# Optimization experiments

Hardware: AMD Instinct MI355X
Metric: run time of the kernel (lower is better)

## Reference

```python
import jax, jax.numpy as jnp
import numpy as np

E = 16        # n_routed_experts
K = 2         # n_activated_experts (top-k)
DIM = 1024    # model dim
INTER = 704   # moe_inter_dim
B, S = 4, 1024


def setup_inputs() -> dict:
    key = jax.random.key(0)
    ks = jax.random.split(key, 5)
    x = jax.random.normal(ks[0], (B, S, DIM), dtype=jnp.float32)
    Wg = jax.random.normal(ks[1], (E, DIM), dtype=jnp.float32) * 0.02   # gate (Linear, no bias)
    W1 = jax.random.normal(ks[2], (E, DIM, INTER), dtype=jnp.float32) * 0.02
    W3 = jax.random.normal(ks[3], (E, DIM, INTER), dtype=jnp.float32) * 0.02
    W2 = jax.random.normal(ks[4], (E, INTER, DIM), dtype=jnp.float32) * 0.02
    return {"x": x, "Wg": Wg, "W1": W1, "W2": W2, "W3": W3}


def reference(x, Wg, W1, W2, W3):
    # Single-process semantics of MoEWithAll2All: the all2all dispatch/combine is
    # pure communication; the math is: softmax router -> top-k -> renormalize ->
    # per-expert SwiGLU MLP on routed tokens -> weighted combine at original slots.
    Bb, Ss, D = x.shape
    xf = x.reshape(-1, D)                              # [N, D], N = B*S
    logits = xf @ Wg.T                                 # [N, E]
    probs = jax.nn.softmax(logits, axis=-1)
    topw, topi = jax.lax.top_k(probs, K)               # [N, K]
    topw = topw / topw.sum(axis=-1, keepdims=True)
    # gates[n, e] = routed weight of token n for expert e (0 if not routed):
    # identical math to the masked gather/scatter dispatch in the original.
    gates = (jax.nn.one_hot(topi, E, dtype=xf.dtype) * topw[..., None]).sum(axis=1)  # [N, E]
    out = jnp.zeros_like(xf)
    for e in range(E):                                 # small fixed loop over experts
        h = jax.nn.silu(xf @ W1[e]) * (xf @ W3[e])     # SwiGLU expert, [N, INTER]
        out = out + gates[:, e:e + 1] * (h @ W2[e])    # combine with gate weights
    return out.reshape(Bb, Ss, D)
```

## Files before the change

### kernel.cpp

```cpp
#include <hip/hip_runtime.h>

#define NTOK 4096
#define DDIM 1024
#define IDIM 704
#define NEXP 16
#define NSLOT 8192
#define MAXT 128
#define NPAD1 768
#define WTBLK 4480

typedef __attribute__((ext_vector_type(8))) short bf16x8;
typedef __attribute__((ext_vector_type(4))) float f32x4;
typedef __attribute__((ext_vector_type(4))) unsigned short us4;
typedef __attribute__((ext_vector_type(8))) unsigned short us8;

__device__ __forceinline__ unsigned short f2bf(float f) {
  union { float f; unsigned int u; } v; v.f = f;
  unsigned int r = v.u + 0x7fffu + ((v.u >> 16) & 1u);
  return (unsigned short)(r >> 16);
}

__device__ __forceinline__ float bf2f(unsigned short b) {
  union { unsigned int u; float f; } v; v.u = ((unsigned int)b) << 16;
  return v.f;
}

__device__ __forceinline__ void gload_lds16(const void* g, void* l) {
  __builtin_amdgcn_global_load_lds((const __attribute__((address_space(1))) void*)g,
                                   (__attribute__((address_space(3))) void*)l, 16, 0, 0);
}

__global__ void k_front(const float* __restrict__ x, const float* __restrict__ Wg,
                        const float* __restrict__ W1, const float* __restrict__ W3,
                        const float* __restrict__ W2, int* __restrict__ tok_e,
                        float* __restrict__ tok_w, unsigned short* __restrict__ Xb,
                        unsigned short* __restrict__ W1T, unsigned short* __restrict__ W3T,
                        unsigned short* __restrict__ W2T) {
  int b = blockIdx.x;
  if (b < WTBLK) {
    __shared__ unsigned short lds[2][64 * 64];
    const float* src; unsigned short* dst;
    int ksz, nsz, kx, np, e;
    if (b < 3072) {
      int which = (b >= 1536) ? 1 : 0;
      int tb = b - which * 1536;
      kx = tb & 15; int rest = tb >> 4; np = rest % 6; e = rest / 6;
      ksz = DDIM; nsz = IDIM;
      src = (which ? W3 : W1) + (size_t)e * DDIM * IDIM;
      dst = (which ? W3T : W1T) + (size_t)e * NPAD1 * DDIM;
    } else {
      int tb = b - 3072;
      kx = tb % 11; int rest = tb / 11; np = rest & 7; e = rest >> 3;
      ksz = IDIM; nsz = DDIM;
      src = W2 + (size_t)e * IDIM * DDIM;
      dst = W2T + (size_t)e * DDIM * IDIM;
    }
    int k0 = kx * 64;
    int t = threadIdx.x;
    int kr4 = (t >> 4) * 4, nc4 = (t & 15) * 4;
    int n0a = np * 128, n0b = n0a + 64;
    bool bvalid = n0b < nsz;
    f32x4 v0[4], v1[4];
#pragma unroll
    for (int j = 0; j < 4; ++j)
      v0[j] = *(const f32x4*)(src + (size_t)(k0 + kr4 + j) * nsz + n0a + nc4);
    if (bvalid) {
#pragma unroll
      for (int j = 0; j < 4; ++j)
        v1[j] = *(const f32x4*)(src + (size_t)(k0 + kr4 + j) * nsz + n0b + nc4);
    }
    int c8 = kr4 >> 3, half = (kr4 >> 2) & 1;
#pragma unroll
    for (int i = 0; i < 4; ++i) {
      int row = nc4 + i;
      int addr = row * 64 + ((c8 ^ ((row >> 2) & 7)) << 3) + half * 4;
      us4 o0;
#pragma unroll
      for (int j = 0; j < 4; ++j) o0[j] = f2bf(v0[j][i]);
      *(us4*)(lds[0] + addr) = o0;
      if (bvalid) {
        us4 o1;
#pragma unroll
        for (int j = 0; j < 4; ++j) o1[j] = f2bf(v1[j][i]);
        *(us4*)(lds[1] + addr) = o1;
      }
    }
    __syncthreads();
    int nr = t >> 3, kc8 = t & 7;
#pragma unroll
    for (int q = 0; q < 2; ++q) {
      int row = nr + q * 32;
      us8 oA = *(const us8*)(lds[0] + row * 64 + ((kc8 ^ ((row >> 2) & 7)) << 3));
      *(us8*)(dst + (size_t)(n0a + row) * ksz + k0 + kc8 * 8) = oA;
      us8 oB = bvalid ? *(const us8*)(lds[1] + row * 64 + ((kc8 ^ ((row >> 2) & 7)) << 3))
                      : (us8)(unsigned short)0;
      *(us8*)(dst + (size_t)(n0b + row) * ksz + k0 + kc8 * 8) = oB;
    }
    return;
  }
  int rb = b - WTBLK;
  int lane = threadIdx.x & 63;
  int wv = threadIdx.x >> 6;
  int tk = rb * 4 + wv;
  const f32x4* xr = (const f32x4*)(x + (size_t)tk * DDIM);
  us4* xbr = (us4*)(Xb + (size_t)tk * DDIM);
  f32x4 xv[4];
#pragma unroll
  for (int c = 0; c < 4; ++c) {
    xv[c] = xr[c * 64 + lane];
    us4 o;
#pragma unroll
    for (int j = 0; j < 4; ++j) o[j] = f2bf(xv[c][j]);
    xbr[c * 64 + lane] = o;
  }
  float p[NEXP];
#pragma unroll
  for (int e = 0; e < NEXP; ++e) {
    const f32x4* wr = (const f32x4*)(Wg + (size_t)e * DDIM);
    float s = 0.f;
#pragma unroll
    for (int c = 0; c < 4; ++c) {
      f32x4 w4 = wr[c * 64 + lane];
      s += xv[c][0]*w4[0] + xv[c][1]*w4[1] + xv[c][2]*w4[2] + xv[c][3]*w4[3];
    }
    p[e] = s;
  }
#pragma unroll
  for (int off = 32; off >= 1; off >>= 1) {
#pragma unroll
    for (int e = 0; e < NEXP; ++e) p[e] += __shfl_xor(p[e], off);
  }
  int i0 = 0; float b0 = p[0];
#pragma unroll
  for (int e = 1; e < NEXP; ++e) if (p[e] > b0) { b0 = p[e]; i0 = e; }
  int i1 = -1; float b1 = -3.4e38f;
#pragma unroll
  for (int e = 0; e < NEXP; ++e) if (e != i0 && p[e] > b1) { b1 = p[e]; i1 = e; }
  if (lane == 0) {
    float w0 = 1.f / (1.f + __expf(b1 - b0));
    tok_e[2*tk] = i0; tok_e[2*tk+1] = i1;
    tok_w[2*tk] = w0; tok_w[2*tk+1] = 1.f - w0;
  }
}

__global__ void k_scan_scatter(const int* __restrict__ tok_e, const float* __restrict__ tok_w,
                               int* __restrict__ counts, int* __restrict__ offsets,
                               int* __restrict__ ntiles, int* __restrict__ tile_e,
                               int* __restrict__ tile_m0, int* __restrict__ token_map,
                               float* __restrict__ gate_w, int* __restrict__ slot_of) {
  int eb = blockIdx.x;
  int t = threadIdx.x, lane = t & 63, wv = t >> 6;
  __shared__ unsigned long long masks[4][32];
  __shared__ int wcnt[4][NEXP];
  __shared__ int counts_s[NEXP];
  int ce[NEXP];
#pragma unroll
  for (int e = 0; e < NEXP; ++e) ce[e] = 0;
#pragma unroll 1
  for (int s = 0; s < 32; ++s) {
    int te = tok_e[wv * 2048 + s * 64 + lane];
#pragma unroll
    for (int e = 0; e < NEXP; ++e) {
      unsigned long long m = __ballot(te == e);
      ce[e] += (int)__popcll(m);
      if (e == eb && lane == 0) masks[wv][s] = m;
    }
  }
  if (lane == 0) {
#pragma unroll
    for (int e = 0; e < NEXP; ++e) wcnt[wv][e] = ce[e];
  }
  __syncthreads();
  if (t < NEXP) {
    int s = wcnt[0][t] + wcnt[1][t] + wcnt[2][t] + wcnt[3][t];
    counts_s[t] = s;
    if (eb == 0) counts[t] = s;
  }
  __syncthreads();
  if (eb == 0 && t == 0) {
    int acc = 0, nt = 0;
    for (int e = 0; e < NEXP; ++e) {
      offsets[e] = acc;
      int cc = counts_s[e];
      for (int m0 = 0; m0 < cc; m0 += 128) { tile_e[nt] = e; tile_m0[nt] = m0; ++nt; }
      acc += cc;
    }
    offsets[NEXP] = acc;
    *ntiles = nt;
  }
  int run = 0;
  for (int e = 0; e < eb; ++e) run += counts_s[e];
  for (int w = 0; w < wv; ++w) run += wcnt[w][eb];
  unsigned long long below = (lane == 63) ? 0x7fffffffffffffffull : ((1ull << lane) - 1ull);
#pragma unroll 1
  for (int s = 0; s < 32; ++s) {
    unsigned long long m = masks[wv][s];
    if ((m >> lane) & 1ull) {
      int i = wv * 2048 + s * 64 + lane;
      int slot = run + (int)__popcll(m & below);
      token_map[slot] = i >> 1;
      gate_w[slot] = tok_w[i];
      slot_of[i] = slot;
    }
    run += (int)__popcll(m);
  }
}

__global__ __launch_bounds__(256, 2)
void k_gemm1(const unsigned short* __restrict__ Xb, const unsigned short* __restrict__ W1T,
             const unsigned short* __restrict__ W3T, const int* __restrict__ token_map,
             const float* __restrict__ gate_w, const int* __restrict__ ntiles,
             const int* __restrict__ tile_e, const int* __restrict__ tile_m0,
             const int* __restrict__ offsets, const int* __restrict__ counts,
             unsigned short* __restrict__ H) {
  int idx = blockIdx.x;
  int xcd = idx & 7, r = idx >> 3;
  int g = (r >> 2) * 8 + xcd;
  int mm = r & 3;
  int ty = (g / 6) * 4 + mm;
  if (ty >= *ntiles) return;
  int n0 = (g % 6) * 128;
  int e = tile_e[ty], m0 = tile_m0[ty];
  int base_slot = offsets[e] + m0;
  int cnt = counts[e] - m0; if (cnt > 128) cnt = 128;

  __shared__ unsigned short As[2][128 * 32];
  __shared__ unsigned short B1s[2][128 * 32];
  __shared__ unsigned short B3s[2][128 * 32];

  int t = threadIdx.x;
  int row = t >> 2, kc = (t & 3) * 8;
  int r0i = base_slot + row;      if (r0i > NSLOT - 1) r0i = NSLOT - 1;
  int r1i = base_slot + 64 + row; if (r1i > NSLOT - 1) r1i = NSLOT - 1;
  const unsigned short* ag0 = Xb + (size_t)token_map[r0i] * DDIM + kc;
  const unsigned short* ag1 = Xb + (size_t)token_map[r1i] * DDIM + kc;
  const unsigned short* b1g0 = W1T + ((size_t)e * NPAD1 + n0 + row) * DDIM + kc;
  const unsigned short* b1g1 = b1g0 + (size_t)64 * DDIM;
  const unsigned short* b3g0 = W3T + ((size_t)e * NPAD1 + n0 + row) * DDIM + kc;
  const unsigned short* b3g1 = b3g0 + (size_t)64 * DDIM;
  int d0 = t * 8, d1 = 2048 + t * 8;

  int lane = t & 63, wv = t >> 6;
  int wm = (wv >> 1) * 64, wn = (wv & 1) * 64;
  int lm = lane & 15, kg = lane >> 4;
  int ao[4], bo[4];
#pragma unroll
  for (int i = 0; i < 4; ++i) {
    ao[i] = (wm + i * 16 + lm) * 32 + kg * 8;
    bo[i] = (wn + i * 16 + lm) * 32 + kg * 8;
  }

  f32x4 acc1[4][4], acc3[4][4];
#pragma unroll
  for (int i = 0; i < 4; ++i)
#pragma unroll
    for (int j = 0; j < 4; ++j) { acc1[i][j] = 0.f; acc3[i][j] = 0.f; }

  gload_lds16(ag0, As[0] + d0);
  gload_lds16(ag1, As[0] + d1);
  gload_lds16(b1g0, B1s[0] + d0);
  gload_lds16(b1g1, B1s[0] + d1);
  gload_lds16(b3g0, B3s[0] + d0);
  gload_lds16(b3g1, B3s[0] + d1);

  for (int k0 = 0; k0 < DDIM; k0 += 32) {
    int cur = (k0 >> 5) & 1;
    __syncthreads();
    if (k0 + 32 < DDIM) {
      int nx = cur ^ 1, kn = k0 + 32;
      gload_lds16(ag0 + kn, As[nx] + d0);
      gload_lds16(ag1 + kn, As[nx] + d1);
      gload_lds16(b1g0 + kn, B1s[nx] + d0);
      gload_lds16(b1g1 + kn, B1s[nx] + d1);
      gload_lds16(b3g0 + kn, B3s[nx] + d0);
      gload_lds16(b3g1 + kn, B3s[nx] + d1);
    }
    bf16x8 av[4], b1v[4], b3v[4];
#pragma unroll
    for (int i = 0; i < 4; ++i) {
      av[i]  = *(const bf16x8*)(As[cur] + ao[i]);
      b1v[i] = *(const bf16x8*)(B1s[cur] + bo[i]);
      b3v[i] = *(const bf16x8*)(B3s[cur] + bo[i]);
    }
#pragma unroll
    for (int mi = 0; mi < 4; ++mi)
#pragma unroll
      for (int ni = 0; ni < 4; ++ni) {
        acc1[mi][ni] = __builtin_amdgcn_mfma_f32_16x16x32_bf16(av[mi], b1v[ni], acc1[mi][ni], 0, 0, 0);
        acc3[mi][ni] = __builtin_amdgcn_mfma_f32_16x16x32_bf16(av[mi], b3v[ni], acc3[mi][ni], 0, 0, 0);
      }
  }

#pragma unroll
  for (int mi = 0; mi < 4; ++mi)
#pragma unroll
    for (int rr = 0; rr < 4; ++rr) {
      int orow = wm + mi * 16 + kg * 4 + rr;
      if (orow < cnt) {
        int slot = base_slot + orow;
        float gw = gate_w[slot];
        unsigned short* hrow = H + (size_t)slot * IDIM;
#pragma unroll
        for (int ni = 0; ni < 4; ++ni) {
          int nn = n0 + wn + ni * 16 + lm;
          if (nn < IDIM) {
            float v1 = acc1[mi][ni][rr];
            float v3 = acc3[mi][ni][rr];
            float hh = v1 / (1.f + __expf(-v1)) * v3 * gw;
            hrow[nn] = f2bf(hh);
          }
        }
      }
    }
}

__global__ __launch_bounds__(256, 3)
void k_gemm2(const unsigned short* __restrict__ H, const unsigned short* __restrict__ W2T,
             const int* __restrict__ ntiles, const int* __restrict__ tile_e,
             const int* __restrict__ tile_m0, const int* __restrict__ offsets,
             const int* __restrict__ counts, unsigned short* __restrict__ O2) {
  int idx = blockIdx.x;
  int xcd = idx & 7, r = idx >> 3;
  int g = (r >> 2) * 8 + xcd;
  int mm = r & 3;
  int ty = (g >> 3) * 4 + mm;
  if (ty >= *ntiles) return;
  int n0 = (g & 7) * 128;
  int e = tile_e[ty], m0 = tile_m0[ty];
  int base_slot = offsets[e] + m0;
  int cnt = counts[e] - m0; if (cnt > 128) cnt = 128;

  __shared__ unsigned short As[2][128 * 32];
  __shared__ unsigned short Bs[2][128 * 32];

  int t = threadIdx.x;
  int row = t >> 2, kc = (t & 3) * 8;
  int r0i = base_slot + row;      if (r0i > NSLOT - 1) r0i = NSLOT - 1;
  int r1i = base_slot + 64 + row; if (r1i > NSLOT - 1) r1i = NSLOT - 1;
  const unsigned short* ag0 = H + (size_t)r0i * IDIM + kc;
  const unsigned short* ag1 = H + (size_t)r1i * IDIM + kc;
  const unsigned short* bg0 = W2T + ((size_t)e * DDIM + n0 + row) * IDIM + kc;
  const unsigned short* bg1 = bg0 + (size_t)64 * IDIM;
  int d0 = t * 8, d1 = 2048 + t * 8;

  int lane = t & 63, wv = t >> 6;
  int wm = (wv >> 1) * 64, wn = (wv & 1) * 64;
  int lm = lane & 15, kg = lane >> 4;
  int ao[4], bo[4];
#pragma unroll
  for (int i = 0; i < 4; ++i) {
    ao[i] = (wm + i * 16 + lm) * 32 + kg * 8;
    bo[i] = (wn + i * 16 + lm) * 32 + kg * 8;
  }

  f32x4 acc[4][4];
#pragma unroll
  for (int i = 0; i < 4; ++i)
#pragma unroll
    for (int j = 0; j < 4; ++j) acc[i][j] = 0.f;

  gload_lds16(ag0, As[0] + d0);
  gload_lds16(ag1, As[0] + d1);
  gload_lds16(bg0, Bs[0] + d0);
  gload_lds16(bg1, Bs[0] + d1);

  for (int k0 = 0; k0 < IDIM; k0 += 32) {
    int cur = (k0 >> 5) & 1;
    __syncthreads();
    if (k0 + 32 < IDIM) {
      int nx = cur ^ 1, kn = k0 + 32;
      gload_lds16(ag0 + kn, As[nx] + d0);
      gload_lds16(ag1 + kn, As[nx] + d1);
      gload_lds16(bg0 + kn, Bs[nx] + d0);
      gload_lds16(bg1 + kn, Bs[nx] + d1);
    }
    bf16x8 av[4], bv[4];
#pragma unroll
    for (int i = 0; i < 4; ++i) {
      av[i] = *(const bf16x8*)(As[cur] + ao[i]);
      bv[i] = *(const bf16x8*)(Bs[cur] + bo[i]);
    }
#pragma unroll
    for (int mi = 0; mi < 4; ++mi)
#pragma unroll
      for (int ni = 0; ni < 4; ++ni)
        acc[mi][ni] = __builtin_amdgcn_mfma_f32_16x16x32_bf16(av[mi], bv[ni], acc[mi][ni], 0, 0, 0);
  }

#pragma unroll
  for (int mi = 0; mi < 4; ++mi)
#pragma unroll
    for (int rr = 0; rr < 4; ++rr) {
      int orow = wm + mi * 16 + kg * 4 + rr;
      if (orow < cnt) {
        unsigned short* op = O2 + (size_t)(base_slot + orow) * DDIM + n0;
#pragma unroll
        for (int ni = 0; ni < 4; ++ni)
          op[wn + ni * 16 + lm] = f2bf(acc[mi][ni][rr]);
      }
    }
}

__global__ void k_combine(const unsigned short* __restrict__ O2, const int* __restrict__ slot_of,
                          float* __restrict__ out) {
  int tk = blockIdx.x, tt = threadIdx.x;
  int s0 = slot_of[2 * tk], s1 = slot_of[2 * tk + 1];
  us4 a = ((const us4*)(O2 + (size_t)s0 * DDIM))[tt];
  us4 b = ((const us4*)(O2 + (size_t)s1 * DDIM))[tt];
  f32x4 o;
#pragma unroll
  for (int j = 0; j < 4; ++j) o[j] = bf2f(a[j]) + bf2f(b[j]);
  ((f32x4*)(out + (size_t)tk * DDIM))[tt] = o;
}

extern "C" void kernel_launch(void* const* d_in, const int* in_sizes, int n_in,
                              void* d_out, int out_size, void* d_ws, size_t ws_size,
                              hipStream_t stream) {
  const float* x  = (const float*)d_in[0];
  const float* Wg = (const float*)d_in[1];
  const float* W1 = (const float*)d_in[2];
  const float* W2 = (const float*)d_in[3];
  const float* W3 = (const float*)d_in[4];
  float* out = (float*)d_out;

  char* ws = (char*)d_ws;
  size_t off = 0;
  unsigned short* Xb = (unsigned short*)(ws + off); off += (size_t)NTOK * DDIM * 2;
  unsigned short* H  = (unsigned short*)(ws + off); off += (size_t)NSLOT * IDIM * 2;
  unsigned short* O2 = (unsigned short*)(ws + off); off += (size_t)NSLOT * DDIM * 2;
  unsigned short* W1T = (unsigned short*)(ws + off); off += (size_t)NEXP * NPAD1 * DDIM * 2;
  unsigned short* W3T = (unsigned short*)(ws + off); off += (size_t)NEXP * NPAD1 * DDIM * 2;
  unsigned short* W2T = (unsigned short*)(ws + off); off += (size_t)NEXP * DDIM * IDIM * 2;
  int* counts  = (int*)(ws + off); off += 64;
  int* offsets = (int*)(ws + off); off += 128;
  int* ntiles  = (int*)(ws + off); off += 64;
  int* tile_e  = (int*)(ws + off); off += MAXT * 4;
  int* tile_m0 = (int*)(ws + off); off += MAXT * 4;
  int* tok_e   = (int*)(ws + off); off += NSLOT * 4;
  float* tok_w = (float*)(ws + off); off += NSLOT * 4;
  int* token_map = (int*)(ws + off); off += NSLOT * 4;
  float* gate_w  = (float*)(ws + off); off += NSLOT * 4;
  int* slot_of   = (int*)(ws + off); off += NSLOT * 4;

  k_front<<<WTBLK + 1024, 256, 0, stream>>>(x, Wg, W1, W3, W2, tok_e, tok_w, Xb,
                                            W1T, W3T, W2T);
  k_scan_scatter<<<NEXP, 256, 0, stream>>>(tok_e, tok_w, counts, offsets, ntiles,
                                           tile_e, tile_m0, token_map, gate_w, slot_of);
  k_gemm1<<<480, 256, 0, stream>>>(Xb, W1T, W3T, token_map, gate_w, ntiles, tile_e,
                                   tile_m0, offsets, counts, H);
  k_gemm2<<<640, 256, 0, stream>>>(H, W2T, ntiles, tile_e, tile_m0, offsets, counts, O2);
  k_combine<<<4096, 256, 0, stream>>>(O2, slot_of, out);
}
```

Before: 297.8 us.

## Widen weight-transpose tiles, route two tokens per wave, bit-ballot expert counting

```diff
diff --git a/kernel.cpp b/kernel.cpp
--- a/kernel.cpp
+++ b/kernel.cpp
@@ -7,7 +7,8 @@
 #define NSLOT 8192
 #define MAXT 128
 #define NPAD1 768
-#define WTBLK 4480
+#define RTRBLK 512
+#define TRBLK 2240
 
 typedef __attribute__((ext_vector_type(8))) short bf16x8;
 typedef __attribute__((ext_vector_type(4))) float f32x4;
@@ -30,116 +31,127 @@
                                    (__attribute__((address_space(3))) void*)l, 16, 0, 0);
 }
 
-__global__ void k_front(const float* __restrict__ x, const float* __restrict__ Wg,
-                        const float* __restrict__ W1, const float* __restrict__ W3,
-                        const float* __restrict__ W2, int* __restrict__ tok_e,
-                        float* __restrict__ tok_w, unsigned short* __restrict__ Xb,
-                        unsigned short* __restrict__ W1T, unsigned short* __restrict__ W3T,
-                        unsigned short* __restrict__ W2T) {
+__global__ __launch_bounds__(256, 4)
+void k_front(const float* __restrict__ x, const float* __restrict__ Wg,
+             const float* __restrict__ W1, const float* __restrict__ W3,
+             const float* __restrict__ W2, int* __restrict__ tok_e,
+             float* __restrict__ tok_w, unsigned short* __restrict__ Xb,
+             unsigned short* __restrict__ W1T, unsigned short* __restrict__ W3T,
+             unsigned short* __restrict__ W2T) {
   int b = blockIdx.x;
-  if (b < WTBLK) {
-    __shared__ unsigned short lds[2][64 * 64];
+  if (b >= RTRBLK) {
+    __shared__ unsigned short lds[4][64 * 64];
+    int tb = b - RTRBLK;
     const float* src; unsigned short* dst;
     int ksz, nsz, kx, np, e;
-    if (b < 3072) {
-      int which = (b >= 1536) ? 1 : 0;
-      int tb = b - which * 1536;
-      kx = tb & 15; int rest = tb >> 4; np = rest % 6; e = rest / 6;
+    if (tb < 1536) {
+      int which = tb >= 768 ? 1 : 0;
+      int t2 = tb - which * 768;
+      kx = t2 & 15; int rest = t2 >> 4; np = rest % 3; e = rest / 3;
       ksz = DDIM; nsz = IDIM;
       src = (which ? W3 : W1) + (size_t)e * DDIM * IDIM;
       dst = (which ? W3T : W1T) + (size_t)e * NPAD1 * DDIM;
     } else {
-      int tb = b - 3072;
-      kx = tb % 11; int rest = tb / 11; np = rest & 7; e = rest >> 3;
+      int t3 = tb - 1536;
+      kx = t3 % 11; int rest = t3 / 11; np = rest & 3; e = rest >> 2;
       ksz = IDIM; nsz = DDIM;
       src = W2 + (size_t)e * IDIM * DDIM;
       dst = W2T + (size_t)e * DDIM * IDIM;
     }
-    int k0 = kx * 64;
+    int k0 = kx * 64, n0 = np * 256;
     int t = threadIdx.x;
     int kr4 = (t >> 4) * 4, nc4 = (t & 15) * 4;
-    int n0a = np * 128, n0b = n0a + 64;
-    bool bvalid = n0b < nsz;
-    f32x4 v0[4], v1[4];
-#pragma unroll
-    for (int j = 0; j < 4; ++j)
-      v0[j] = *(const f32x4*)(src + (size_t)(k0 + kr4 + j) * nsz + n0a + nc4);
-    if (bvalid) {
-#pragma unroll
-      for (int j = 0; j < 4; ++j)
-        v1[j] = *(const f32x4*)(src + (size_t)(k0 + kr4 + j) * nsz + n0b + nc4);
+    f32x4 v[4][4];
+    bool val[4];
+#pragma unroll
+    for (int s = 0; s < 4; ++s) {
+      val[s] = (n0 + s * 64 + 64) <= nsz;
+      if (val[s]) {
+#pragma unroll
+        for (int j = 0; j < 4; ++j)
+          v[s][j] = *(const f32x4*)(src + (size_t)(k0 + kr4 + j) * nsz + n0 + s * 64 + nc4);
+      }
     }
     int c8 = kr4 >> 3, half = (kr4 >> 2) & 1;
 #pragma unroll
-    for (int i = 0; i < 4; ++i) {
-      int row = nc4 + i;
-      int addr = row * 64 + ((c8 ^ ((row >> 2) & 7)) << 3) + half * 4;
-      us4 o0;
-#pragma unroll
-      for (int j = 0; j < 4; ++j) o0[j] = f2bf(v0[j][i]);
-      *(us4*)(lds[0] + addr) = o0;
-      if (bvalid) {
-        us4 o1;
-#pragma unroll
-        for (int j = 0; j < 4; ++j) o1[j] = f2bf(v1[j][i]);
-        *(us4*)(lds[1] + addr) = o1;
+    for (int s = 0; s < 4; ++s) {
+      if (val[s]) {
+#pragma unroll
+        for (int i = 0; i < 4; ++i) {
+          int row = nc4 + i;
+          int addr = row * 64 + ((c8 ^ ((row >> 2) & 7)) << 3) + half * 4;
+          us4 o;
+#pragma unroll
+          for (int j = 0; j < 4; ++j) o[j] = f2bf(v[s][j][i]);
+          *(us4*)(lds[s] + addr) = o;
+        }
       }
     }
     __syncthreads();
     int nr = t >> 3, kc8 = t & 7;
 #pragma unroll
-    for (int q = 0; q < 2; ++q) {
-      int row = nr + q * 32;
-      us8 oA = *(const us8*)(lds[0] + row * 64 + ((kc8 ^ ((row >> 2) & 7)) << 3));
-      *(us8*)(dst + (size_t)(n0a + row) * ksz + k0 + kc8 * 8) = oA;
-      us8 oB = bvalid ? *(const us8*)(lds[1] + row * 64 + ((kc8 ^ ((row >> 2) & 7)) << 3))
-                      : (us8)(unsigned short)0;
-      *(us8*)(dst + (size_t)(n0b + row) * ksz + k0 + kc8 * 8) = oB;
+    for (int s = 0; s < 4; ++s) {
+#pragma unroll
+      for (int q = 0; q < 2; ++q) {
+        int row = nr + q * 32;
+        us8 o = val[s] ? *(const us8*)(lds[s] + row * 64 + ((kc8 ^ ((row >> 2) & 7)) << 3))
+                       : (us8)(unsigned short)0;
+        *(us8*)(dst + (size_t)(n0 + s * 64 + row) * ksz + k0 + kc8 * 8) = o;
+      }
     }
     return;
   }
-  int rb = b - WTBLK;
   int lane = threadIdx.x & 63;
   int wv = threadIdx.x >> 6;
-  int tk = rb * 4 + wv;
-  const f32x4* xr = (const f32x4*)(x + (size_t)tk * DDIM);
-  us4* xbr = (us4*)(Xb + (size_t)tk * DDIM);
-  f32x4 xv[4];
-#pragma unroll
-  for (int c = 0; c < 4; ++c) {
-    xv[c] = xr[c * 64 + lane];
-    us4 o;
-#pragma unroll
-    for (int j = 0; j < 4; ++j) o[j] = f2bf(xv[c][j]);
-    xbr[c * 64 + lane] = o;
-  }
-  float p[NEXP];
+  int tk0 = b * 8 + wv * 2;
+  f32x4 xv[2][4];
+#pragma unroll
+  for (int tok = 0; tok < 2; ++tok) {
+    const f32x4* xr = (const f32x4*)(x + (size_t)(tk0 + tok) * DDIM);
+    us4* xbr = (us4*)(Xb + (size_t)(tk0 + tok) * DDIM);
+#pragma unroll
+    for (int c = 0; c < 4; ++c) {
+      xv[tok][c] = xr[c * 64 + lane];
+      us4 o;
+#pragma unroll
+      for (int j = 0; j < 4; ++j) o[j] = f2bf(xv[tok][c][j]);
+      xbr[c * 64 + lane] = o;
+    }
+  }
+  float p[2][NEXP];
 #pragma unroll
   for (int e = 0; e < NEXP; ++e) {
     const f32x4* wr = (const f32x4*)(Wg + (size_t)e * DDIM);
-    float s = 0.f;
+    float s0 = 0.f, s1 = 0.f;
 #pragma unroll
     for (int c = 0; c < 4; ++c) {
       f32x4 w4 = wr[c * 64 + lane];
-      s += xv[c][0]*w4[0] + xv[c][1]*w4[1] + xv[c][2]*w4[2] + xv[c][3]*w4[3];
-    }
-    p[e] = s;
-  }
-#pragma unroll
-  for (int off = 32; off >= 1; off >>= 1) {
-#pragma unroll
-    for (int e = 0; e < NEXP; ++e) p[e] += __shfl_xor(p[e], off);
-  }
-  int i0 = 0; float b0 = p[0];
-#pragma unroll
-  for (int e = 1; e < NEXP; ++e) if (p[e] > b0) { b0 = p[e]; i0 = e; }
-  int i1 = -1; float b1 = -3.4e38f;
-#pragma unroll
-  for (int e = 0; e < NEXP; ++e) if (e != i0 && p[e] > b1) { b1 = p[e]; i1 = e; }
-  if (lane == 0) {
-    float w0 = 1.f / (1.f + __expf(b1 - b0));
-    tok_e[2*tk] = i0; tok_e[2*tk+1] = i1;
-    tok_w[2*tk] = w0; tok_w[2*tk+1] = 1.f - w0;
+      s0 += xv[0][c][0]*w4[0] + xv[0][c][1]*w4[1] + xv[0][c][2]*w4[2] + xv[0][c][3]*w4[3];
+      s1 += xv[1][c][0]*w4[0] + xv[1][c][1]*w4[1] + xv[1][c][2]*w4[2] + xv[1][c][3]*w4[3];
+    }
+    p[0][e] = s0; p[1][e] = s1;
+  }
+#pragma unroll
+  for (int off = 32; off >= 1; off >>= 1)
+#pragma unroll
+    for (int e = 0; e < NEXP; ++e) {
+      p[0][e] += __shfl_xor(p[0][e], off);
+      p[1][e] += __shfl_xor(p[1][e], off);
+    }
+#pragma unroll
+  for (int tok = 0; tok < 2; ++tok) {
+    int i0 = 0; float b0 = p[tok][0];
+#pragma unroll
+    for (int e = 1; e < NEXP; ++e) if (p[tok][e] > b0) { b0 = p[tok][e]; i0 = e; }
+    int i1 = -1; float b1 = -3.4e38f;
+#pragma unroll
+    for (int e = 0; e < NEXP; ++e) if (e != i0 && p[tok][e] > b1) { b1 = p[tok][e]; i1 = e; }
+    if (lane == 0) {
+      int tk = tk0 + tok;
+      float w0 = 1.f / (1.f + __expf(b1 - b0));
+      tok_e[2*tk] = i0; tok_e[2*tk+1] = i1;
+      tok_w[2*tk] = w0; tok_w[2*tk+1] = 1.f - w0;
+    }
   }
 }
 
@@ -156,15 +168,23 @@
   int ce[NEXP];
 #pragma unroll
   for (int e = 0; e < NEXP; ++e) ce[e] = 0;
+  int base = wv * 2048 + lane;
+  int te = tok_e[base];
 #pragma unroll 1
   for (int s = 0; s < 32; ++s) {
-    int te = tok_e[wv * 2048 + s * 64 + lane];
+    int ten = (s < 31) ? tok_e[base + (s + 1) * 64] : 0;
+    unsigned long long B0 = __ballot(te & 1);
+    unsigned long long B1 = __ballot(te & 2);
+    unsigned long long B2 = __ballot(te & 4);
+    unsigned long long B3 = __ballot(te & 8);
 #pragma unroll
     for (int e = 0; e < NEXP; ++e) {
-      unsigned long long m = __ballot(te == e);
+      unsigned long long m = ((e & 1) ? B0 : ~B0) & ((e & 2) ? B1 : ~B1) &
+                             ((e & 4) ? B2 : ~B2) & ((e & 8) ? B3 : ~B3);
       ce[e] += (int)__popcll(m);
       if (e == eb && lane == 0) masks[wv][s] = m;
     }
+    te = ten;
   }
   if (lane == 0) {
 #pragma unroll
@@ -442,8 +462,8 @@
   float* gate_w  = (float*)(ws + off); off += NSLOT * 4;
   int* slot_of   = (int*)(ws + off); off += NSLOT * 4;
 
-  k_front<<<WTBLK + 1024, 256, 0, stream>>>(x, Wg, W1, W3, W2, tok_e, tok_w, Xb,
-                                            W1T, W3T, W2T);
+  k_front<<<RTRBLK + TRBLK, 256, 0, stream>>>(x, Wg, W1, W3, W2, tok_e, tok_w, Xb,
+                                              W1T, W3T, W2T);
   k_scan_scatter<<<NEXP, 256, 0, stream>>>(tok_e, tok_w, counts, offsets, ntiles,
                                            tile_e, tile_m0, token_map, gate_w, slot_of);
   k_gemm1<<<480, 256, 0, stream>>>(Xb, W1T, W3T, token_map, gate_w, ntiles, tile_e,
```

After: 305.5 us. +2.6%, slower.
